# Kernel tuning notes

Measured on AMD Instinct MI355X. Metric: run time of the kernel, lower is better.

Reference implementation:

```python
import jax, jax.numpy as jnp
import numpy as np

KH = KW = 3
STRIDE = 1
PAD = 1
DIL = 1

def setup_inputs() -> dict:
    key = jax.random.key(0)
    k1, k2, k3, k4, k5 = jax.random.split(key, 5)
    B, C, H, W = 8, 256, 64, 64
    O = 256
    inp = jax.random.normal(k1, (B, C, H, W), dtype=jnp.float32)
    offset = jax.random.normal(k2, (B, 2 * KH * KW, H, W), dtype=jnp.float32)
    mask = jax.random.uniform(k3, (B, KH * KW, H, W), dtype=jnp.float32)
    weight = jax.random.normal(k4, (O, C, KH, KW), dtype=jnp.float32) * (1.0 / np.sqrt(C * KH * KW))
    bias = jax.random.normal(k5, (O,), dtype=jnp.float32) * 0.01
    return {"input": inp, "offset": offset, "mask": mask, "weight": weight, "bias": bias}


def _gather(img_flat, idx):
    # img_flat: [C, H*W], idx: [K2, Ho, Wo] -> [C, K2, Ho, Wo]
    return img_flat[:, idx]


def _deform_conv2d(inp, offset, mask, weight, bias):
    B, C, H, W = inp.shape
    O = weight.shape[0]
    K2 = KH * KW
    Ho = (H + 2 * PAD - DIL * (KH - 1) - 1) // STRIDE + 1
    Wo = (W + 2 * PAD - DIL * (KW - 1) - 1) // STRIDE + 1

    # offset layout: channel 2*k is dy, 2*k+1 is dx for kernel tap k
    off = offset.reshape(B, K2, 2, Ho, Wo)
    off_y, off_x = off[:, :, 0], off[:, :, 1]  # [B, K2, Ho, Wo]

    ki = (jnp.arange(K2) // KW) * DIL  # kernel row offset per tap
    kj = (jnp.arange(K2) % KW) * DIL   # kernel col offset per tap
    base_y = (jnp.arange(Ho) * STRIDE - PAD)[None, :, None] + ki[:, None, None]  # [K2,Ho,1]
    base_x = (jnp.arange(Wo) * STRIDE - PAD)[None, None, :] + kj[:, None, None]  # [K2,1,Wo]

    y = off_y + base_y[None]  # [B, K2, Ho, Wo]
    x = off_x + base_x[None]

    y0 = jnp.floor(y)
    x0 = jnp.floor(x)
    ly = y - y0
    lx = x - x0
    hy = 1.0 - ly
    hx = 1.0 - lx
    y0i = y0.astype(jnp.int32)
    x0i = x0.astype(jnp.int32)

    img_flat = inp.reshape(B, C, H * W)

    def corner(yy, xx, w):
        valid = (yy >= 0) & (yy < H) & (xx >= 0) & (xx < W)
        idx = jnp.clip(yy, 0, H - 1) * W + jnp.clip(xx, 0, W - 1)  # [B,K2,Ho,Wo]
        vals = jax.vmap(_gather)(img_flat, idx)  # [B,C,K2,Ho,Wo]
        wgt = jnp.where(valid, w, 0.0)[:, None]  # [B,1,K2,Ho,Wo]
        return vals * wgt

    sampled = (corner(y0i, x0i, hy * hx)
               + corner(y0i, x0i + 1, hy * lx)
               + corner(y0i + 1, x0i, ly * hx)
               + corner(y0i + 1, x0i + 1, ly * lx))  # [B,C,K2,Ho,Wo]

    sampled = sampled * mask[:, None]  # modulated deformable conv v2

    w2 = weight.reshape(O, C, K2)
    out = jnp.einsum('bckhw,ock->bohw', sampled, w2) + bias[None, :, None, None]
    return out


def reference(input, offset, mask, weight, bias):
    return _deform_conv2d(input, offset, mask, weight, bias)
```

## Files before the change

kernel.cpp:

```cpp
#include <hip/hip_runtime.h>

typedef _Float16 f16x8 __attribute__((ext_vector_type(8)));
typedef float    f32x4 __attribute__((ext_vector_type(4)));

namespace {
constexpr int Bb = 8, Cc = 256, Oo = 256;
constexpr int HW = 4096;
constexpr int NCH2 = 36;
constexpr int SROW2 = 72;
constexpr int TBLK = 512;
}

__device__ inline f16x8 sp8(_Float16 x) { f16x8 r = {x,x,x,x,x,x,x,x}; return r; }

__device__ __forceinline__ void barrier_lgkm() {
  asm volatile("s_waitcnt lgkmcnt(0)" ::: "memory");
  __builtin_amdgcn_s_barrier();
}

__global__ __launch_bounds__(256)
void prep(const float* __restrict__ in, const float* __restrict__ w,
          _Float16* __restrict__ outh, _Float16* __restrict__ wh) {
  const int bid = blockIdx.x;
  const int t   = threadIdx.x;
  if (bid < TBLK) {
    const int b = bid >> 6, pxg = bid & 63;
    const int c8 = t & 31, pxq = t >> 5;
    const float* src = in + (size_t)b * Cc * HW + pxg * 64 + pxq * 8;
    float4 va[8], vb[8];
#pragma unroll
    for (int k = 0; k < 8; ++k) {
      const float* s = src + (size_t)(c8 * 8 + k) * HW;
      va[k] = *(const float4*)(s);
      vb[k] = *(const float4*)(s + 4);
    }
    _Float16* dst = outh + ((size_t)b * HW + pxg * 64 + pxq * 8) * Cc + c8 * 8;
#pragma unroll
    for (int p = 0; p < 4; ++p) {
      f16x8 o0, o1;
#pragma unroll
      for (int k = 0; k < 8; ++k) {
        float a = (p == 0) ? va[k].x : (p == 1) ? va[k].y : (p == 2) ? va[k].z : va[k].w;
        float bq = (p == 0) ? vb[k].x : (p == 1) ? vb[k].y : (p == 2) ? vb[k].z : vb[k].w;
        o0[k] = (_Float16)a;
        o1[k] = (_Float16)bq;
      }
      *(f16x8*)(dst + (size_t)p * Cc)       = o0;
      *(f16x8*)(dst + (size_t)(p + 4) * Cc) = o1;
    }
  } else {
    int tt = (bid - TBLK) * 256 + t;
    int o  = tt & 255;
    int Kb = (tt >> 8) * 8;
    const float* s = w + (size_t)o * 2304;
    f16x8 v;
#pragma unroll
    for (int k8 = 0; k8 < 8; ++k8) {
      int K = Kb + k8;
      int tap = K >> 8, c = K & 255;
      v[k8] = (_Float16)s[c * 9 + tap];
    }
    *(f16x8*)(wh + (size_t)tt * 8) = v;
  }
}

__global__ __launch_bounds__(512, 2)
void dcn_mfma(const _Float16* __restrict__ inh,
              const _Float16* __restrict__ wgh,
              const float* __restrict__ offset,
              const float* __restrict__ mask,
              const float* __restrict__ bias,
              float* __restrict__ out) {
  __shared__ __align__(16) _Float16 Sl[2][128 * SROW2];

  const int tid = threadIdx.x;
  const int b   = blockIdx.x;
  const int rp  = blockIdx.y;

  const int pos = tid >> 2, cg = tid & 3;
  const int ho  = rp * 2 + (pos >> 6), wo = pos & 63;
  const int lane = tid & 63, wm = tid >> 6;
  const int lq = lane >> 4, lr = lane & 15;

  const f16x8* gin = (const f16x8*)(inh + (size_t)b * HW * Cc);
  const uint4* wg4 = (const uint4*)wgh;
  const int    wbase = lq * 256 + wm * 32 + lr;

  int4   mi_c, mi_n = {0,0,0,0};
  float4 mwt_c, mwt_n = {0,0,0,0};
  float  ofy, ofx, msk;
  f16x8  vc[2][8];
  uint4  awv[4];

  auto load_md_inputs = [&](int tap) {
    ofy = offset[(((size_t)b * 18 + 2 * tap)     * 64 + ho) * 64 + wo];
    ofx = offset[(((size_t)b * 18 + 2 * tap + 1) * 64 + ho) * 64 + wo];
    msk = mask  [(((size_t)b * 9  + tap)         * 64 + ho) * 64 + wo];
  };
  auto build_md = [&](int tap, int4& mio, float4& mwo) {
    int ki = tap / 3, kj = tap % 3;
    float y = ofy + (float)(ho - 1 + ki);
    float x = ofx + (float)(wo - 1 + kj);
    float y0f = floorf(y), x0f = floorf(x);
    float ly = y - y0f, lx = x - x0f;
    float hy = 1.f - ly, hx = 1.f - lx;
    int y0 = (int)y0f, x0 = (int)x0f;
    int y1 = y0 + 1, x1 = x0 + 1;
    bool vy0 = (unsigned)y0 < 64u, vy1 = (unsigned)y1 < 64u;
    bool vx0 = (unsigned)x0 < 64u, vx1 = (unsigned)x1 < 64u;
    int cy0 = min(max(y0, 0), 63), cy1 = min(max(y1, 0), 63);
    int cx0 = min(max(x0, 0), 63), cx1 = min(max(x1, 0), 63);
    mwo.x = (vy0 && vx0) ? hy * hx * msk : 0.f;
    mwo.y = (vy0 && vx1) ? hy * lx * msk : 0.f;
    mwo.z = (vy1 && vx0) ? ly * hx * msk : 0.f;
    mwo.w = (vy1 && vx1) ? ly * lx * msk : 0.f;
    mio = make_int4(cy0 * 64 + cx0, cy0 * 64 + cx1, cy1 * 64 + cx0, cy1 * 64 + cx1);
  };
  auto gather = [&](const int4& m, int cc, f16x8* dst) {
    int cb = (cc & 3) * 8 + cg;
    dst[0] = gin[m.x * 32 + cb];     dst[1] = gin[m.y * 32 + cb];
    dst[2] = gin[m.z * 32 + cb];     dst[3] = gin[m.w * 32 + cb];
    dst[4] = gin[m.x * 32 + cb + 4]; dst[5] = gin[m.y * 32 + cb + 4];
    dst[6] = gin[m.z * 32 + cb + 4]; dst[7] = gin[m.w * 32 + cb + 4];
  };
  auto stage = [&](const f16x8* v, const float4& w, int buf) {
    f16x8 s0 = v[0] * sp8((_Float16)w.x) + v[1] * sp8((_Float16)w.y)
             + v[2] * sp8((_Float16)w.z) + v[3] * sp8((_Float16)w.w);
    f16x8 s1 = v[4] * sp8((_Float16)w.x) + v[5] * sp8((_Float16)w.y)
             + v[6] * sp8((_Float16)w.z) + v[7] * sp8((_Float16)w.w);
    *(f16x8*)(&Sl[buf][pos * SROW2 + cg * 8])      = s0;
    *(f16x8*)(&Sl[buf][pos * SROW2 + 32 + cg * 8]) = s1;
  };
  auto wload_half = [&](int cc, int h) {
    const uint4* base = wg4 + (size_t)(2 * cc + h) * 1024 + wbase;
#pragma unroll
    for (int mt = 0; mt < 2; ++mt) awv[h * 2 + mt] = base[mt * 16];
  };

  f32x4 acc[2][8];
#pragma unroll
  for (int mt = 0; mt < 2; ++mt)
#pragma unroll
    for (int nt = 0; nt < 8; ++nt) {
      acc[mt][nt][0] = 0.f; acc[mt][nt][1] = 0.f;
      acc[mt][nt][2] = 0.f; acc[mt][nt][3] = 0.f;
    }

  load_md_inputs(0);
  build_md(0, mi_c, mwt_c);
  gather(mi_c, 0, vc[0]);
  wload_half(0, 0); wload_half(0, 1);
  gather(mi_c, 1, vc[1]);
  stage(vc[0], mwt_c, 0);
  barrier_lgkm();

  for (int t = 0; t < 9; ++t) {
#pragma unroll
    for (int j = 0; j < 4; ++j) {
      const int cc  = t * 4 + j;
      const int cur = j & 1;

      if (j < 2) {
        gather(mi_c, cc + 2, vc[cur]);
      } else if (t < 8) {
        if (j == 2) build_md(t + 1, mi_n, mwt_n);
        gather(mi_n, cc + 2, vc[cur]);
      }
      if (j == 0 && t < 8) load_md_inputs(t + 1);

      {
        f16x8 afr[2];
#pragma unroll
        for (int mt = 0; mt < 2; ++mt) afr[mt] = __builtin_bit_cast(f16x8, awv[mt]);
        if (cc + 1 < NCH2) wload_half(cc + 1, 0);
#pragma unroll
        for (int nt = 0; nt < 8; ++nt) {
          f16x8 bfr = *(const f16x8*)(&Sl[cur][(nt * 16 + lr) * SROW2 + lq * 8]);
#pragma unroll
          for (int mt = 0; mt < 2; ++mt)
            acc[mt][nt] = __builtin_amdgcn_mfma_f32_16x16x32_f16(afr[mt], bfr, acc[mt][nt], 0, 0, 0);
        }
      }
      {
        f16x8 afr[2];
#pragma unroll
        for (int mt = 0; mt < 2; ++mt) afr[mt] = __builtin_bit_cast(f16x8, awv[2 + mt]);
        if (cc + 1 < NCH2) wload_half(cc + 1, 1);
#pragma unroll
        for (int nt = 0; nt < 8; ++nt) {
          f16x8 bfr = *(const f16x8*)(&Sl[cur][(nt * 16 + lr) * SROW2 + 32 + lq * 8]);
#pragma unroll
          for (int mt = 0; mt < 2; ++mt)
            acc[mt][nt] = __builtin_amdgcn_mfma_f32_16x16x32_f16(afr[mt], bfr, acc[mt][nt], 0, 0, 0);
        }
      }

      if (j < 3) {
        stage(vc[cur ^ 1], mwt_c, cur ^ 1);
      } else if (t < 8) {
        stage(vc[cur ^ 1], mwt_n, cur ^ 1);
      }
      barrier_lgkm();
    }
    if (t < 8) { mi_c = mi_n; mwt_c = mwt_n; }
  }

#pragma unroll
  for (int mt = 0; mt < 2; ++mt) {
#pragma unroll
    for (int reg = 0; reg < 4; ++reg) {
      int o = wm * 32 + mt * 16 + lq * 4 + reg;
      float bv = bias[o];
      float* op = out + ((size_t)(b * 256 + o)) * 4096 + rp * 128 + lr;
#pragma unroll
      for (int nt = 0; nt < 8; ++nt)
        op[nt * 16] = acc[mt][nt][reg] + bv;
    }
  }
}

extern "C" void kernel_launch(void* const* d_in, const int* in_sizes, int n_in,
                              void* d_out, int out_size, void* d_ws, size_t ws_size,
                              hipStream_t stream) {
  const float* inp    = (const float*)d_in[0];
  const float* offset = (const float*)d_in[1];
  const float* mask   = (const float*)d_in[2];
  const float* weight = (const float*)d_in[3];
  const float* bias   = (const float*)d_in[4];
  float* out = (float*)d_out;

  _Float16* inh = (_Float16*)d_ws;
  _Float16* wgh = inh + (size_t)Bb * HW * Cc;

  hipLaunchKernelGGL(prep, dim3(TBLK + 288), dim3(256), 0, stream,
                     inp, weight, inh, wgh);
  hipLaunchKernelGGL(dcn_mfma, dim3(Bb, 32), dim3(512), 0, stream,
                     inh, wgh, offset, mask, bias, out);
}
```

Baseline: 145.2 us.

## Fuse prep and deformable conv into one cooperative kernel with grid sync

Merges the fp16 conversion and transpose kernel into the main MFMA kernel, which is now launched cooperatively as 256 blocks of 512 threads. A grid-wide sync separates the conversion phase from the compute phase. The block-to-(batch, row-pair) mapping changes from a 2D grid to a linearised index. This removes one kernel launch and the gap between kernels, at the cost of a grid barrier and a conversion phase that runs on fewer, larger blocks.

```diff
diff --git a/kernel.cpp b/kernel.cpp
--- a/kernel.cpp
+++ b/kernel.cpp
@@ -1,4 +1,7 @@
 #include <hip/hip_runtime.h>
+#include <hip/hip_cooperative_groups.h>
+
+namespace cg = cooperative_groups;
 
 typedef _Float16 f16x8 __attribute__((ext_vector_type(8)));
 typedef float    f32x4 __attribute__((ext_vector_type(4)));
@@ -8,7 +11,6 @@
 constexpr int HW = 4096;
 constexpr int NCH2 = 36;
 constexpr int SROW2 = 72;
-constexpr int TBLK = 512;
 }
 
 __device__ inline f16x8 sp8(_Float16 x) { f16x8 r = {x,x,x,x,x,x,x,x}; return r; }
@@ -18,14 +20,39 @@
   __builtin_amdgcn_s_barrier();
 }
 
-__global__ __launch_bounds__(256)
-void prep(const float* __restrict__ in, const float* __restrict__ w,
-          _Float16* __restrict__ outh, _Float16* __restrict__ wh) {
-  const int bid = blockIdx.x;
-  const int t   = threadIdx.x;
-  if (bid < TBLK) {
-    const int b = bid >> 6, pxg = bid & 63;
-    const int c8 = t & 31, pxq = t >> 5;
+__global__ __launch_bounds__(512, 2)
+void dcn_fused(const float* __restrict__ in,
+               const float* __restrict__ w,
+               _Float16* __restrict__ inh,
+               _Float16* __restrict__ wgh,
+               const float* __restrict__ offset,
+               const float* __restrict__ mask,
+               const float* __restrict__ bias,
+               float* __restrict__ out) {
+  __shared__ __align__(16) _Float16 Sl[2][128 * SROW2];
+
+  const int tid  = threadIdx.x;
+  const int bidx = blockIdx.x;
+
+  {
+    const int g = bidx * 512 + tid;
+    if (g < 73728) {
+      int o  = g & 255;
+      int Kb = (g >> 8) * 8;
+      const float* s = w + (size_t)o * 2304;
+      f16x8 v;
+#pragma unroll
+      for (int k8 = 0; k8 < 8; ++k8) {
+        int K = Kb + k8;
+        int tap = K >> 8, c = K & 255;
+        v[k8] = (_Float16)s[c * 9 + tap];
+      }
+      *(f16x8*)(wgh + (size_t)g * 8) = v;
+    }
+    const int bt = g >> 8;
+    const int tt = g & 255;
+    const int b  = bt >> 6, pxg = bt & 63;
+    const int c8 = tt & 31, pxq = tt >> 5;
     const float* src = in + (size_t)b * Cc * HW + pxg * 64 + pxq * 8;
     float4 va[8], vb[8];
 #pragma unroll
@@ -34,13 +61,13 @@
       va[k] = *(const float4*)(s);
       vb[k] = *(const float4*)(s + 4);
     }
-    _Float16* dst = outh + ((size_t)b * HW + pxg * 64 + pxq * 8) * Cc + c8 * 8;
+    _Float16* dst = inh + ((size_t)b * HW + pxg * 64 + pxq * 8) * Cc + c8 * 8;
 #pragma unroll
     for (int p = 0; p < 4; ++p) {
       f16x8 o0, o1;
 #pragma unroll
       for (int k = 0; k < 8; ++k) {
-        float a = (p == 0) ? va[k].x : (p == 1) ? va[k].y : (p == 2) ? va[k].z : va[k].w;
+        float a  = (p == 0) ? va[k].x : (p == 1) ? va[k].y : (p == 2) ? va[k].z : va[k].w;
         float bq = (p == 0) ? vb[k].x : (p == 1) ? vb[k].y : (p == 2) ? vb[k].z : vb[k].w;
         o0[k] = (_Float16)a;
         o1[k] = (_Float16)bq;
@@ -48,36 +75,14 @@
       *(f16x8*)(dst + (size_t)p * Cc)       = o0;
       *(f16x8*)(dst + (size_t)(p + 4) * Cc) = o1;
     }
-  } else {
-    int tt = (bid - TBLK) * 256 + t;
-    int o  = tt & 255;
-    int Kb = (tt >> 8) * 8;
-    const float* s = w + (size_t)o * 2304;
-    f16x8 v;
-#pragma unroll
-    for (int k8 = 0; k8 < 8; ++k8) {
-      int K = Kb + k8;
-      int tap = K >> 8, c = K & 255;
-      v[k8] = (_Float16)s[c * 9 + tap];
-    }
-    *(f16x8*)(wh + (size_t)tt * 8) = v;
   }
-}
-
-__global__ __launch_bounds__(512, 2)
-void dcn_mfma(const _Float16* __restrict__ inh,
-              const _Float16* __restrict__ wgh,
-              const float* __restrict__ offset,
-              const float* __restrict__ mask,
-              const float* __restrict__ bias,
-              float* __restrict__ out) {
-  __shared__ __align__(16) _Float16 Sl[2][128 * SROW2];
-
-  const int tid = threadIdx.x;
-  const int b   = blockIdx.x;
-  const int rp  = blockIdx.y;
-
-  const int pos = tid >> 2, cg = tid & 3;
+
+  cg::this_grid().sync();
+
+  const int b   = bidx & 7;
+  const int rp  = bidx >> 3;
+
+  const int pos = tid >> 2, cg_ = tid & 3;
   const int ho  = rp * 2 + (pos >> 6), wo = pos & 63;
   const int lane = tid & 63, wm = tid >> 6;
   const int lq = lane >> 4, lr = lane & 15;
@@ -117,19 +122,19 @@
     mio = make_int4(cy0 * 64 + cx0, cy0 * 64 + cx1, cy1 * 64 + cx0, cy1 * 64 + cx1);
   };
   auto gather = [&](const int4& m, int cc, f16x8* dst) {
-    int cb = (cc & 3) * 8 + cg;
+    int cb = (cc & 3) * 8 + cg_;
     dst[0] = gin[m.x * 32 + cb];     dst[1] = gin[m.y * 32 + cb];
     dst[2] = gin[m.z * 32 + cb];     dst[3] = gin[m.w * 32 + cb];
     dst[4] = gin[m.x * 32 + cb + 4]; dst[5] = gin[m.y * 32 + cb + 4];
     dst[6] = gin[m.z * 32 + cb + 4]; dst[7] = gin[m.w * 32 + cb + 4];
   };
-  auto stage = [&](const f16x8* v, const float4& w, int buf) {
-    f16x8 s0 = v[0] * sp8((_Float16)w.x) + v[1] * sp8((_Float16)w.y)
-             + v[2] * sp8((_Float16)w.z) + v[3] * sp8((_Float16)w.w);
-    f16x8 s1 = v[4] * sp8((_Float16)w.x) + v[5] * sp8((_Float16)w.y)
-             + v[6] * sp8((_Float16)w.z) + v[7] * sp8((_Float16)w.w);
-    *(f16x8*)(&Sl[buf][pos * SROW2 + cg * 8])      = s0;
-    *(f16x8*)(&Sl[buf][pos * SROW2 + 32 + cg * 8]) = s1;
+  auto stage = [&](const f16x8* v, const float4& wv, int buf) {
+    f16x8 s0 = v[0] * sp8((_Float16)wv.x) + v[1] * sp8((_Float16)wv.y)
+             + v[2] * sp8((_Float16)wv.z) + v[3] * sp8((_Float16)wv.w);
+    f16x8 s1 = v[4] * sp8((_Float16)wv.x) + v[5] * sp8((_Float16)wv.y)
+             + v[6] * sp8((_Float16)wv.z) + v[7] * sp8((_Float16)wv.w);
+    *(f16x8*)(&Sl[buf][pos * SROW2 + cg_ * 8])      = s0;
+    *(f16x8*)(&Sl[buf][pos * SROW2 + 32 + cg_ * 8]) = s1;
   };
   auto wload_half = [&](int cc, int h) {
     const uint4* base = wg4 + (size_t)(2 * cc + h) * 1024 + wbase;
@@ -232,8 +237,8 @@
   _Float16* inh = (_Float16*)d_ws;
   _Float16* wgh = inh + (size_t)Bb * HW * Cc;
 
-  hipLaunchKernelGGL(prep, dim3(TBLK + 288), dim3(256), 0, stream,
-                     inp, weight, inh, wgh);
-  hipLaunchKernelGGL(dcn_mfma, dim3(Bb, 32), dim3(512), 0, stream,
-                     inh, wgh, offset, mask, bias, out);
-}
+  void* args[] = { (void*)&inp, (void*)&weight, (void*)&inh, (void*)&wgh,
+                   (void*)&offset, (void*)&mask, (void*)&bias, (void*)&out };
+  hipLaunchCooperativeKernel((const void*)dcn_fused,
+                             dim3(256), dim3(512), args, 0, stream);
+}
```

After: 198.3 us. 1.37x slower.

## Use triple-buffered LDS staging to cut register pressure and raise occupancy

Applied to the files above, without the earlier changes.

The gather/stage pipeline moves from two in-flight register buffers plus a double-buffered LDS tile to a single register gather buffer and a three-slot LDS ring. Each gathered chunk is staged into LDS two chunks ahead, so the next-tap metadata no longer has to be kept alive alongside the current one. This frees VGPRs, and the launch bound is raised to target 4 blocks per CU. The trade-off is more LDS per block and less latency hiding in registers, since each global gather now has to complete within one iteration before it is staged.

```diff
diff --git a/kernel.cpp b/kernel.cpp
--- a/kernel.cpp
+++ b/kernel.cpp
@@ -40,7 +40,7 @@
       f16x8 o0, o1;
 #pragma unroll
       for (int k = 0; k < 8; ++k) {
-        float a = (p == 0) ? va[k].x : (p == 1) ? va[k].y : (p == 2) ? va[k].z : va[k].w;
+        float a  = (p == 0) ? va[k].x : (p == 1) ? va[k].y : (p == 2) ? va[k].z : va[k].w;
         float bq = (p == 0) ? vb[k].x : (p == 1) ? vb[k].y : (p == 2) ? vb[k].z : vb[k].w;
         o0[k] = (_Float16)a;
         o1[k] = (_Float16)bq;
@@ -64,14 +64,14 @@
   }
 }
 
-__global__ __launch_bounds__(512, 2)
+__global__ __launch_bounds__(512, 4)
 void dcn_mfma(const _Float16* __restrict__ inh,
               const _Float16* __restrict__ wgh,
               const float* __restrict__ offset,
               const float* __restrict__ mask,
               const float* __restrict__ bias,
               float* __restrict__ out) {
-  __shared__ __align__(16) _Float16 Sl[2][128 * SROW2];
+  __shared__ __align__(16) _Float16 Sl[3][128 * SROW2];
 
   const int tid = threadIdx.x;
   const int b   = blockIdx.x;
@@ -86,10 +86,10 @@
   const uint4* wg4 = (const uint4*)wgh;
   const int    wbase = lq * 256 + wm * 32 + lr;
 
-  int4   mi_c, mi_n = {0,0,0,0};
-  float4 mwt_c, mwt_n = {0,0,0,0};
+  int4   mi_c = {0,0,0,0};
+  float4 mwt_c = {0,0,0,0};
   float  ofy, ofx, msk;
-  f16x8  vc[2][8];
+  f16x8  vc[8];
   uint4  awv[4];
 
   auto load_md_inputs = [&](int tap) {
@@ -97,7 +97,7 @@
     ofx = offset[(((size_t)b * 18 + 2 * tap + 1) * 64 + ho) * 64 + wo];
     msk = mask  [(((size_t)b * 9  + tap)         * 64 + ho) * 64 + wo];
   };
-  auto build_md = [&](int tap, int4& mio, float4& mwo) {
+  auto build_md = [&](int tap) {
     int ki = tap / 3, kj = tap % 3;
     float y = ofy + (float)(ho - 1 + ki);
     float x = ofx + (float)(wo - 1 + kj);
@@ -110,24 +110,24 @@
     bool vx0 = (unsigned)x0 < 64u, vx1 = (unsigned)x1 < 64u;
     int cy0 = min(max(y0, 0), 63), cy1 = min(max(y1, 0), 63);
     int cx0 = min(max(x0, 0), 63), cx1 = min(max(x1, 0), 63);
-    mwo.x = (vy0 && vx0) ? hy * hx * msk : 0.f;
-    mwo.y = (vy0 && vx1) ? hy * lx * msk : 0.f;
-    mwo.z = (vy1 && vx0) ? ly * hx * msk : 0.f;
-    mwo.w = (vy1 && vx1) ? ly * lx * msk : 0.f;
-    mio = make_int4(cy0 * 64 + cx0, cy0 * 64 + cx1, cy1 * 64 + cx0, cy1 * 64 + cx1);
-  };
-  auto gather = [&](const int4& m, int cc, f16x8* dst) {
+    mwt_c.x = (vy0 && vx0) ? hy * hx * msk : 0.f;
+    mwt_c.y = (vy0 && vx1) ? hy * lx * msk : 0.f;
+    mwt_c.z = (vy1 && vx0) ? ly * hx * msk : 0.f;
+    mwt_c.w = (vy1 && vx1) ? ly * lx * msk : 0.f;
+    mi_c = make_int4(cy0 * 64 + cx0, cy0 * 64 + cx1, cy1 * 64 + cx0, cy1 * 64 + cx1);
+  };
+  auto gather = [&](int cc) {
     int cb = (cc & 3) * 8 + cg;
-    dst[0] = gin[m.x * 32 + cb];     dst[1] = gin[m.y * 32 + cb];
-    dst[2] = gin[m.z * 32 + cb];     dst[3] = gin[m.w * 32 + cb];
-    dst[4] = gin[m.x * 32 + cb + 4]; dst[5] = gin[m.y * 32 + cb + 4];
-    dst[6] = gin[m.z * 32 + cb + 4]; dst[7] = gin[m.w * 32 + cb + 4];
-  };
-  auto stage = [&](const f16x8* v, const float4& w, int buf) {
-    f16x8 s0 = v[0] * sp8((_Float16)w.x) + v[1] * sp8((_Float16)w.y)
-             + v[2] * sp8((_Float16)w.z) + v[3] * sp8((_Float16)w.w);
-    f16x8 s1 = v[4] * sp8((_Float16)w.x) + v[5] * sp8((_Float16)w.y)
-             + v[6] * sp8((_Float16)w.z) + v[7] * sp8((_Float16)w.w);
+    vc[0] = gin[mi_c.x * 32 + cb];     vc[1] = gin[mi_c.y * 32 + cb];
+    vc[2] = gin[mi_c.z * 32 + cb];     vc[3] = gin[mi_c.w * 32 + cb];
+    vc[4] = gin[mi_c.x * 32 + cb + 4]; vc[5] = gin[mi_c.y * 32 + cb + 4];
+    vc[6] = gin[mi_c.z * 32 + cb + 4]; vc[7] = gin[mi_c.w * 32 + cb + 4];
+  };
+  auto stage = [&](int buf) {
+    f16x8 s0 = vc[0] * sp8((_Float16)mwt_c.x) + vc[1] * sp8((_Float16)mwt_c.y)
+             + vc[2] * sp8((_Float16)mwt_c.z) + vc[3] * sp8((_Float16)mwt_c.w);
+    f16x8 s1 = vc[4] * sp8((_Float16)mwt_c.x) + vc[5] * sp8((_Float16)mwt_c.y)
+             + vc[6] * sp8((_Float16)mwt_c.z) + vc[7] * sp8((_Float16)mwt_c.w);
     *(f16x8*)(&Sl[buf][pos * SROW2 + cg * 8])      = s0;
     *(f16x8*)(&Sl[buf][pos * SROW2 + 32 + cg * 8]) = s1;
   };
@@ -147,26 +147,27 @@
     }
 
   load_md_inputs(0);
-  build_md(0, mi_c, mwt_c);
-  gather(mi_c, 0, vc[0]);
+  build_md(0);
+  gather(0);
   wload_half(0, 0); wload_half(0, 1);
-  gather(mi_c, 1, vc[1]);
-  stage(vc[0], mwt_c, 0);
+  stage(0);
+  gather(1);
+  stage(1);
   barrier_lgkm();
 
-  for (int t = 0; t < 9; ++t) {
-#pragma unroll
-    for (int j = 0; j < 4; ++j) {
-      const int cc  = t * 4 + j;
-      const int cur = j & 1;
-
-      if (j < 2) {
-        gather(mi_c, cc + 2, vc[cur]);
-      } else if (t < 8) {
-        if (j == 2) build_md(t + 1, mi_n, mwt_n);
-        gather(mi_n, cc + 2, vc[cur]);
-      }
-      if (j == 0 && t < 8) load_md_inputs(t + 1);
+  for (int u = 0; u < 12; ++u) {
+#pragma unroll
+    for (int j = 0; j < 3; ++j) {
+      const int cc = u * 3 + j;
+      const int c2 = cc + 2;
+      const int rd = j;
+      const int wr = (j + 2) % 3;
+
+      if (c2 < NCH2) {
+        if ((c2 & 3) == 0) build_md(c2 >> 2);
+        gather(c2);
+      }
+      if ((c2 & 3) == 2 && c2 < 34) load_md_inputs((c2 + 2) >> 2);
 
       {
         f16x8 afr[2];
@@ -175,7 +176,7 @@
         if (cc + 1 < NCH2) wload_half(cc + 1, 0);
 #pragma unroll
         for (int nt = 0; nt < 8; ++nt) {
-          f16x8 bfr = *(const f16x8*)(&Sl[cur][(nt * 16 + lr) * SROW2 + lq * 8]);
+          f16x8 bfr = *(const f16x8*)(&Sl[rd][(nt * 16 + lr) * SROW2 + lq * 8]);
 #pragma unroll
           for (int mt = 0; mt < 2; ++mt)
             acc[mt][nt] = __builtin_amdgcn_mfma_f32_16x16x32_f16(afr[mt], bfr, acc[mt][nt], 0, 0, 0);
@@ -188,21 +189,16 @@
         if (cc + 1 < NCH2) wload_half(cc + 1, 1);
 #pragma unroll
         for (int nt = 0; nt < 8; ++nt) {
-          f16x8 bfr = *(const f16x8*)(&Sl[cur][(nt * 16 + lr) * SROW2 + 32 + lq * 8]);
+          f16x8 bfr = *(const f16x8*)(&Sl[rd][(nt * 16 + lr) * SROW2 + 32 + lq * 8]);
 #pragma unroll
           for (int mt = 0; mt < 2; ++mt)
             acc[mt][nt] = __builtin_amdgcn_mfma_f32_16x16x32_f16(afr[mt], bfr, acc[mt][nt], 0, 0, 0);
         }
       }
 
-      if (j < 3) {
-        stage(vc[cur ^ 1], mwt_c, cur ^ 1);
-      } else if (t < 8) {
-        stage(vc[cur ^ 1], mwt_n, cur ^ 1);
-      }
+      if (c2 < NCH2) stage(wr);
       barrier_lgkm();
     }
-    if (t < 8) { mi_c = mi_n; mwt_c = mwt_n; }
   }
 
 #pragma unroll
```

Result: slower. 231.2 us (+59.2%).
